# Optimization experiments

Hardware: AMD Instinct MI355X
Metric: run time of the kernel (lower is better)

Reference implementation:

```python
import jax, jax.numpy as jnp
import numpy as np

IN_DIM = 256
OUT_DIM = 256
EMBED_DIM = 256
GROUPS = 8
BN_EPS = 1e-5


def conv2d(x, w, b, pad, groups=1):
    # x: NCHW, w: OIHW (I = in_ch / groups)
    out = jax.lax.conv_general_dilated(
        x, w, window_strides=(1, 1), padding=[(pad, pad), (pad, pad)],
        dimension_numbers=('NCHW', 'OIHW', 'NCHW'), feature_group_count=groups)
    return out + b[None, :, None, None]


def setup_inputs() -> dict:
    key = jax.random.key(0)
    ks = jax.random.split(key, 8)
    s = 0.05
    d = {}
    d['x'] = jax.random.normal(ks[0], (2, IN_DIM, 16, 16), jnp.float32)
    d['y'] = jax.random.normal(ks[1], (2, OUT_DIM, 128, 128), jnp.float32)
    # channle_reduce: Conv2d(256, 64, k=3, groups=64) -> weight (64, 4, 3, 3)
    d['w_cr'] = jax.random.normal(ks[2], (IN_DIM // 4, 4, 3, 3), jnp.float32) * s
    d['b_cr'] = jnp.zeros((IN_DIM // 4,), jnp.float32)
    # depthwise convs on 64 channels
    d['w_dw3'] = jax.random.normal(ks[3], (IN_DIM // 4, 1, 3, 3), jnp.float32) * s
    d['b_dw3'] = jnp.zeros((IN_DIM // 4,), jnp.float32)
    d['w_dw7'] = jax.random.normal(ks[4], (IN_DIM // 4, 1, 5, 5), jnp.float32) * s
    d['b_dw7'] = jnp.zeros((IN_DIM // 4,), jnp.float32)
    # gate: Conv2d(256, 128, 1) + BN + StarReLU
    d['w_gate'] = jax.random.normal(ks[5], (IN_DIM // 2, IN_DIM, 1, 1), jnp.float32) * s
    d['b_gate'] = jnp.zeros((IN_DIM // 2,), jnp.float32)
    d['bn_gamma'] = jnp.ones((IN_DIM // 2,), jnp.float32)
    d['bn_beta'] = jnp.zeros((IN_DIM // 2,), jnp.float32)
    d['bn_mean'] = jnp.zeros((IN_DIM // 2,), jnp.float32)
    d['bn_var'] = jnp.ones((IN_DIM // 2,), jnp.float32)
    d['sr_scale'] = jnp.ones((1,), jnp.float32)
    d['sr_bias'] = jnp.zeros((1,), jnp.float32)
    # linear1: Linear(16, 8192) -> torch weight shape (8192, 16)
    d['w_lin'] = jax.random.normal(ks[6], (OUT_DIM * EMBED_DIM // GROUPS, IN_DIM // (2 * GROUPS)), jnp.float32) * s
    d['b_lin'] = jnp.zeros((OUT_DIM * EMBED_DIM // GROUPS,), jnp.float32)
    return d


def reference(x, y, w_cr, b_cr, w_dw3, b_dw3, w_dw7, b_dw7, w_gate, b_gate,
              bn_gamma, bn_beta, bn_mean, bn_var, sr_scale, sr_bias, w_lin, b_lin):
    B, C, H, Wd = x.shape
    # gate branch: 1x1 conv -> BN (inference stats) -> StarReLU
    g = conv2d(x, w_gate, b_gate, 0)
    inv = (bn_gamma / jnp.sqrt(bn_var + BN_EPS))[None, :, None, None]
    g = (g - bn_mean[None, :, None, None]) * inv + bn_beta[None, :, None, None]
    g = sr_scale * jnp.square(jnp.maximum(g, 0.0)) + sr_bias
    # feature branch
    xr = conv2d(x, w_cr, b_cr, 1, groups=IN_DIM // 4)        # (B, 64, H, W)
    x3 = conv2d(xr, w_dw3, b_dw3, 1, groups=IN_DIM // 4)
    x7 = conv2d(xr, w_dw7, b_dw7, 2, groups=IN_DIM // 4)
    xc = jnp.concatenate([x3, x7], axis=1) * g               # (B, 128, H, W)
    # per-pixel weight generation: (B,H,W,G,16) @ (16,8192)
    xc = xc.reshape(B, GROUPS, -1, H, Wd).transpose(0, 3, 4, 1, 2)
    wdec = jnp.einsum('bhwgi,oi->bhwgo', xc, w_lin) + b_lin  # (B,H,W,8,8192)
    # flatten (G, out*embed/G) -> (embed, out); matches torch reshape order
    wdec = wdec.reshape(B, H, Wd, EMBED_DIM, OUT_DIM)
    # patch-wise dynamic 1x1 conv == per-patch batched matmul
    b, c, h, w = y.shape
    fh, fw = H, Wd
    ph, pw = h // fh, w // fw
    yp = y.reshape(b, c, fh, ph, fw, pw)
    # out[b,e,f,p,g,q] = sum_c wdec[b,f,g,e,c] * y[b,c,f,p,g,q]
    out = jnp.einsum('bfgec,bcfpgq->befpgq', wdec, yp)
    return out.reshape(b, EMBED_DIM, h, w)
```

## Files before the change

### kernel.cpp

```cpp
#include <hip/hip_runtime.h>
#include <stdint.h>


typedef __attribute__((ext_vector_type(8))) short short8;
typedef __attribute__((ext_vector_type(4))) float f32x4;

#define BN_EPS 1e-5f

__device__ __forceinline__ unsigned short f2bf(float f) {
  unsigned u = __float_as_uint(f);
  return (unsigned short)((u + 0x8000u) >> 16);
}
__device__ __forceinline__ unsigned pk2bf(float a, float b) {
  unsigned ua = __float_as_uint(a), ub = __float_as_uint(b);
  return ((ua + 0x8000u) >> 16) | ((ub + 0x8000u) & 0xFFFF0000u);
}

__global__ __launch_bounds__(256) void k1_merged(
    const float* __restrict__ x, const float* __restrict__ w_cr,
    const float* __restrict__ b_cr, const float* __restrict__ w_dw3,
    const float* __restrict__ b_dw3, const float* __restrict__ w_dw7,
    const float* __restrict__ b_dw7, const float* __restrict__ w_gate,
    const float* __restrict__ b_gate, const float* __restrict__ bn_gamma,
    const float* __restrict__ bn_beta, const float* __restrict__ bn_mean,
    const float* __restrict__ bn_var, const float* __restrict__ sr_scale,
    const float* __restrict__ sr_bias, const float* __restrict__ w_lin,
    short* __restrict__ wlin_bf, float* __restrict__ f0_out,
    float* __restrict__ gs_out)
{
  __shared__ __align__(16) float xcen[256];
  __shared__ __align__(16) float xs[4][256];
  __shared__ __align__(16) float xrs[256];

  int blk = blockIdx.x;
  int t = threadIdx.x;

  if (blk < 512) {
    int b = blk >> 8, h = (blk >> 4) & 15, w = blk & 15;
    int pix = (b * 16 + h) * 16 + w;

    { int idx = blk * 256 + t; wlin_bf[idx] = (short)f2bf(w_lin[idx]); }

    xcen[t] = x[b * 65536 + t * 256 + h * 16 + w];
    __syncthreads();

    int wave = t >> 6, lane = t & 63;
    int oq = lane >> 2, ol = lane & 3;
    const float4* wg4 = (const float4*)w_gate;
    const float4* xc4 = (const float4*)xcen;
    float ss = sr_scale[0], sb = sr_bias[0];

    #pragma unroll
    for (int pass = 0; pass < 2; ++pass) {
      int o = wave * 32 + pass * 16 + oq;
      float acc = 0.f;
      #pragma unroll
      for (int k = 0; k < 16; ++k) {
        int j = k * 4 + ol;
        float4 wv = wg4[o * 64 + j];
        float4 xv = xc4[j];
        acc += wv.x * xv.x + wv.y * xv.y + wv.z * xv.z + wv.w * xv.w;
      }
      acc += __shfl_xor(acc, 1);
      acc += __shfl_xor(acc, 2);
      float inv = bn_gamma[o] * rsqrtf(bn_var[o] + BN_EPS);
      float gg = (acc + b_gate[o] - bn_mean[o]) * inv + bn_beta[o];
      gg = fmaxf(gg, 0.f);
      gg = ss * gg * gg + sb;
      if (ol == 0) gs_out[pix * 128 + o] = gg;
    }
  } else {
    int cb = blk - 512;
    int b = cb >> 6, cr = cb & 63;
    {
      int ch = t >> 6, off = (t & 63) * 4;
      float4 v = *(const float4*)(x + b * 65536 + (cr * 4 + ch) * 256 + off);
      *(float4*)&xs[ch][off] = v;
    }
    __syncthreads();
    int h = t >> 4, w = t & 15;
    float a = b_cr[cr];
    #pragma unroll
    for (int ii = 0; ii < 4; ++ii) {
      const float* wp = w_cr + (cr * 4 + ii) * 9;
      #pragma unroll
      for (int ky = 0; ky < 3; ++ky) {
        int gy = h + ky - 1;
        #pragma unroll
        for (int kx = 0; kx < 3; ++kx) {
          int gx = w + kx - 1;
          float v = (gy >= 0 && gy < 16 && gx >= 0 && gx < 16) ? xs[ii][gy * 16 + gx] : 0.f;
          a += wp[ky * 3 + kx] * v;
        }
      }
    }
    xrs[t] = a;
    __syncthreads();

    float f3 = b_dw3[cr];
    {
      const float* wp = w_dw3 + cr * 9;
      #pragma unroll
      for (int ky = 0; ky < 3; ++ky) {
        int gy = h + ky - 1;
        #pragma unroll
        for (int kx = 0; kx < 3; ++kx) {
          int gx = w + kx - 1;
          float v = (gy >= 0 && gy < 16 && gx >= 0 && gx < 16) ? xrs[gy * 16 + gx] : 0.f;
          f3 += wp[ky * 3 + kx] * v;
        }
      }
    }
    float f5 = b_dw7[cr];
    {
      const float* wp = w_dw7 + cr * 25;
      #pragma unroll
      for (int ky = 0; ky < 5; ++ky) {
        int gy = h + ky - 2;
        #pragma unroll
        for (int kx = 0; kx < 5; ++kx) {
          int gx = w + kx - 2;
          float v = (gy >= 0 && gy < 16 && gx >= 0 && gx < 16) ? xrs[gy * 16 + gx] : 0.f;
          f5 += wp[ky * 5 + kx] * v;
        }
      }
    }
    int pix = (b * 16 + h) * 16 + w;
    f0_out[pix * 128 + cr] = f3;
    f0_out[pix * 128 + 64 + cr] = f5;
  }
}

__global__ __launch_bounds__(512, 4) void k2_fused(
    const float* __restrict__ y, const short* __restrict__ wlin_bf,
    const float* __restrict__ f0_in, const float* __restrict__ gs_in,
    const float* __restrict__ b_lin, float* __restrict__ out)
{
  __shared__ __align__(16) short Ylds[16384];
  __shared__ __align__(16) char dyn[16640];
  float* scratch = (float*)dyn;
  short* wdbase = (short*)dyn;

  int phys = blockIdx.x;
  int blk = (phys & 7) * 64 + (phys >> 3);
  int b = blk >> 8, f = (blk >> 4) & 15, g = blk & 15;
  int tid = threadIdx.x;
  int wave = tid >> 6, lane = tid & 63;
  int quad = lane >> 4, l16 = lane & 15;
  int geff = l16 & 7, jsel = l16 >> 3;

  const float* yb = y + b * 4194304 + (f * 8) * 128 + g * 8;

  int c32 = tid >> 4, pf = tid & 15;
  float4 yv[2][2];
  #pragma unroll
  for (int s = 0; s < 2; ++s)
    #pragma unroll
    for (int it = 0; it < 2; ++it)
      yv[s][it] = *(const float4*)(yb + (s * 64 + it * 32 + c32) * 16384 + (pf >> 1) * 128 + (pf & 1) * 4);

  short8 aw[2][2][2];
  float4 bl[2][2][2];
  #pragma unroll
  for (int s = 0; s < 2; ++s)
    #pragma unroll
    for (int jj = 0; jj < 2; ++jj) {
      int jA = wave * 4 + jj * 2 + (quad >> 1);
      int jD = wave * 4 + jj * 2 + jsel;
      #pragma unroll
      for (int hh = 0; hh < 2; ++hh) {
        int c0 = s * 32 + hh * 16;
        aw[s][jj][hh] = *(const short8*)(wlin_bf + (jA * 256 + c0 + l16) * 16 + (quad & 1) * 8);
        bl[s][jj][hh] = *(const float4*)(b_lin + jD * 256 + c0 + quad * 4);
      }
    }

  bool bval = (jsel == (quad >> 1));
  const float* f0p = f0_in + blk * 128 + geff * 16 + (quad & 1) * 8;
  const float* gsp = gs_in + blk * 128 + geff * 16 + (quad & 1) * 8;
  float4 f0a = *(const float4*)f0p, f0b = *(const float4*)(f0p + 4);
  float4 gsa = *(const float4*)gsp, gsb = *(const float4*)(gsp + 4);

  #pragma unroll
  for (int sch = 0; sch < 4; ++sch) {
    #pragma unroll
    for (int it = 0; it < 2; ++it)
      *(float4*)&scratch[(it * 32 + c32) * 65 + pf * 4] = yv[sch & 1][it];
    if (sch < 2) {
      #pragma unroll
      for (int it = 0; it < 2; ++it)
        yv[sch & 1][it] = *(const float4*)(yb + ((sch + 2) * 64 + it * 32 + c32) * 16384 + (pf >> 1) * 128 + (pf & 1) * 4);
    }
    __syncthreads();
    {
      int pix = tid & 63, cg = tid >> 6;
      float s0 = scratch[(cg * 8 + 0) * 65 + pix];
      float s1 = scratch[(cg * 8 + 1) * 65 + pix];
      float s2 = scratch[(cg * 8 + 2) * 65 + pix];
      float s3 = scratch[(cg * 8 + 3) * 65 + pix];
      float s4 = scratch[(cg * 8 + 4) * 65 + pix];
      float s5 = scratch[(cg * 8 + 5) * 65 + pix];
      float s6 = scratch[(cg * 8 + 6) * 65 + pix];
      float s7 = scratch[(cg * 8 + 7) * 65 + pix];
      uint4 pk;
      pk.x = pk2bf(s0, s1); pk.y = pk2bf(s2, s3);
      pk.z = pk2bf(s4, s5); pk.w = pk2bf(s6, s7);
      int chunk = sch * 8 + cg;
      int physc = chunk ^ (pix & 15);
      *(uint4*)&Ylds[pix * 256 + physc * 8] = pk;
    }
    __syncthreads();
  }

  short8 bx = {0, 0, 0, 0, 0, 0, 0, 0};
  if (bval) {
    bx[0] = (short)f2bf(f0a.x * gsa.x); bx[1] = (short)f2bf(f0a.y * gsa.y);
    bx[2] = (short)f2bf(f0a.z * gsa.z); bx[3] = (short)f2bf(f0a.w * gsa.w);
    bx[4] = (short)f2bf(f0b.x * gsb.x); bx[5] = (short)f2bf(f0b.y * gsb.y);
    bx[6] = (short)f2bf(f0b.z * gsb.z); bx[7] = (short)f2bf(f0b.w * gsb.w);
  }

  f32x4 acc[2][4];
  #pragma unroll
  for (int et = 0; et < 2; ++et)
    #pragma unroll
    for (int nt = 0; nt < 4; ++nt)
      acc[et][nt] = {0.f, 0.f, 0.f, 0.f};

  short* wdw = wdbase + wave * 1024;

  auto gen_chunk = [&](int cc, int slot) {
    #pragma unroll
    for (int jj = 0; jj < 2; ++jj) {
      int ep = geff * 4 + jj * 2 + jsel;
      int gx = ((ep >> 2) & 3) ^ (ep & 3);
      #pragma unroll
      for (int hh = 0; hh < 2; ++hh) {
        float4 blv = bl[slot][jj][hh];
        f32x4 cin = {blv.x, blv.y, blv.z, blv.w};
        f32x4 d = __builtin_amdgcn_mfma_f32_16x16x32_bf16(aw[slot][jj][hh], bx, cin, 0, 0, 0);
        uint2 pk;
        pk.x = pk2bf(d[0], d[1]);
        pk.y = pk2bf(d[2], d[3]);
        int q16 = (hh * 2 + (quad >> 1)) ^ gx;
        *(uint2*)&wdw[ep * 32 + q16 * 8 + (quad & 1) * 4] = pk;
      }
    }
  };

  gen_chunk(0, 0);

  #pragma unroll
  for (int cc = 0; cc < 8; ++cc) {
    short8 A2[2], Bf[4];
    #pragma unroll
    for (int et = 0; et < 2; ++et) {
      int ep = (l16 & 7) * 4 + et * 2 + (l16 >> 3);
      int gx = ((ep >> 2) & 3) ^ (ep & 3);
      A2[et] = *(const short8*)&wdw[ep * 32 + (quad ^ gx) * 8];
    }
    int chunkY = cc * 4 + quad;
    #pragma unroll
    for (int nt = 0; nt < 4; ++nt) {
      int physc = chunkY ^ l16;
      Bf[nt] = *(const short8*)&Ylds[(nt * 16 + l16) * 256 + physc * 8];
    }
    if (cc < 6) {
      #pragma unroll
      for (int jj = 0; jj < 2; ++jj) {
        int jA = wave * 4 + jj * 2 + (quad >> 1);
        int jD = wave * 4 + jj * 2 + jsel;
        #pragma unroll
        for (int hh = 0; hh < 2; ++hh) {
          int c0 = (cc + 2) * 32 + hh * 16;
          aw[cc & 1][jj][hh] = *(const short8*)(wlin_bf + (jA * 256 + c0 + l16) * 16 + (quad & 1) * 8);
          bl[cc & 1][jj][hh] = *(const float4*)(b_lin + jD * 256 + c0 + quad * 4);
        }
      }
    }
    if (cc < 7) gen_chunk(cc + 1, (cc + 1) & 1);
    #pragma unroll
    for (int et = 0; et < 2; ++et)
      #pragma unroll
      for (int nt = 0; nt < 4; ++nt)
        acc[et][nt] = __builtin_amdgcn_mfma_f32_16x16x32_bf16(A2[et], Bf[nt], acc[et][nt], 0, 0, 0);
  }

  float* ob = out + b * 4194304 + (f * 8) * 128 + g * 8;
  #pragma unroll
  for (int et = 0; et < 2; ++et) {
    #pragma unroll
    for (int nt = 0; nt < 4; ++nt) {
      int pix = nt * 16 + l16;
      float* oa = ob + (pix >> 3) * 128 + (pix & 7);
      #pragma unroll
      for (int r = 0; r < 4; ++r) {
        int m = quad * 4 + r;
        int e = (m & 7) * 32 + wave * 4 + et * 2 + (m >> 3);
        oa[e * 16384] = acc[et][nt][r];
      }
    }
  }
}

extern "C" void kernel_launch(void* const* d_in, const int* in_sizes, int n_in,
                              void* d_out, int out_size, void* d_ws, size_t ws_size,
                              hipStream_t stream) {
  const float* x        = (const float*)d_in[0];
  const float* y        = (const float*)d_in[1];
  const float* w_cr     = (const float*)d_in[2];
  const float* b_cr     = (const float*)d_in[3];
  const float* w_dw3    = (const float*)d_in[4];
  const float* b_dw3    = (const float*)d_in[5];
  const float* w_dw7    = (const float*)d_in[6];
  const float* b_dw7    = (const float*)d_in[7];
  const float* w_gate   = (const float*)d_in[8];
  const float* b_gate   = (const float*)d_in[9];
  const float* bn_gamma = (const float*)d_in[10];
  const float* bn_beta  = (const float*)d_in[11];
  const float* bn_mean  = (const float*)d_in[12];
  const float* bn_var   = (const float*)d_in[13];
  const float* sr_scale = (const float*)d_in[14];
  const float* sr_bias  = (const float*)d_in[15];
  const float* w_lin    = (const float*)d_in[16];
  const float* b_lin    = (const float*)d_in[17];
  float* out = (float*)d_out;

  float* f0      = (float*)d_ws;
  float* gs      = (float*)((char*)d_ws + 262144);
  short* wlin_bf = (short*)((char*)d_ws + 524288);

  hipLaunchKernelGGL(k1_merged, dim3(640), dim3(256), 0, stream,
                     x, w_cr, b_cr, w_dw3, b_dw3, w_dw7, b_dw7, w_gate, b_gate,
                     bn_gamma, bn_beta, bn_mean, bn_var, sr_scale, sr_bias,
                     w_lin, wlin_bf, f0, gs);
  hipLaunchKernelGGL(k2_fused, dim3(512), dim3(512), 0, stream,
                     y, wlin_bf, f0, gs, b_lin, out);
}
```

Baseline: 152.6 us.

## Fuse prologue convs and gate into main kernel, convert w_lin to bf16 on the fly

Merges the first kernel (grouped conv, depthwise convs, gate conv with BN and StarReLU, w_lin bf16 conversion) into the main per-patch kernel. Each block now recomputes its own pixel's features from a 7x7 halo window of x held in LDS, and converts w_lin from fp32 to bf16 in registers just before each MFMA. This removes a kernel launch and the workspace round trip. In exchange it adds redundant per-block prologue compute, several extra barriers, twice as many bytes loaded for w_lin, and more register pressure.

New measurement: 183.8 us. 20.4% more time.

```diff
diff --git a/kernel.cpp b/kernel.cpp
--- a/kernel.cpp
+++ b/kernel.cpp
@@ -15,151 +15,153 @@
   unsigned ua = __float_as_uint(a), ub = __float_as_uint(b);
   return ((ua + 0x8000u) >> 16) | ((ub + 0x8000u) & 0xFFFF0000u);
 }
-
-__global__ __launch_bounds__(256) void k1_merged(
-    const float* __restrict__ x, const float* __restrict__ w_cr,
-    const float* __restrict__ b_cr, const float* __restrict__ w_dw3,
-    const float* __restrict__ b_dw3, const float* __restrict__ w_dw7,
-    const float* __restrict__ b_dw7, const float* __restrict__ w_gate,
-    const float* __restrict__ b_gate, const float* __restrict__ bn_gamma,
-    const float* __restrict__ bn_beta, const float* __restrict__ bn_mean,
-    const float* __restrict__ bn_var, const float* __restrict__ sr_scale,
-    const float* __restrict__ sr_bias, const float* __restrict__ w_lin,
-    short* __restrict__ wlin_bf, float* __restrict__ f0_out,
-    float* __restrict__ gs_out)
-{
-  __shared__ __align__(16) float xcen[256];
-  __shared__ __align__(16) float xs[4][256];
-  __shared__ __align__(16) float xrs[256];
-
-  int blk = blockIdx.x;
-  int t = threadIdx.x;
-
-  if (blk < 512) {
-    int b = blk >> 8, h = (blk >> 4) & 15, w = blk & 15;
-    int pix = (b * 16 + h) * 16 + w;
-
-    { int idx = blk * 256 + t; wlin_bf[idx] = (short)f2bf(w_lin[idx]); }
-
-    xcen[t] = x[b * 65536 + t * 256 + h * 16 + w];
-    __syncthreads();
-
-    int wave = t >> 6, lane = t & 63;
-    int oq = lane >> 2, ol = lane & 3;
-    const float4* wg4 = (const float4*)w_gate;
-    const float4* xc4 = (const float4*)xcen;
-    float ss = sr_scale[0], sb = sr_bias[0];
-
-    #pragma unroll
-    for (int pass = 0; pass < 2; ++pass) {
-      int o = wave * 32 + pass * 16 + oq;
-      float acc = 0.f;
-      #pragma unroll
-      for (int k = 0; k < 16; ++k) {
-        int j = k * 4 + ol;
-        float4 wv = wg4[o * 64 + j];
-        float4 xv = xc4[j];
-        acc += wv.x * xv.x + wv.y * xv.y + wv.z * xv.z + wv.w * xv.w;
-      }
-      acc += __shfl_xor(acc, 1);
-      acc += __shfl_xor(acc, 2);
-      float inv = bn_gamma[o] * rsqrtf(bn_var[o] + BN_EPS);
-      float gg = (acc + b_gate[o] - bn_mean[o]) * inv + bn_beta[o];
-      gg = fmaxf(gg, 0.f);
-      gg = ss * gg * gg + sb;
-      if (ol == 0) gs_out[pix * 128 + o] = gg;
-    }
-  } else {
-    int cb = blk - 512;
-    int b = cb >> 6, cr = cb & 63;
-    {
-      int ch = t >> 6, off = (t & 63) * 4;
-      float4 v = *(const float4*)(x + b * 65536 + (cr * 4 + ch) * 256 + off);
-      *(float4*)&xs[ch][off] = v;
-    }
-    __syncthreads();
-    int h = t >> 4, w = t & 15;
-    float a = b_cr[cr];
-    #pragma unroll
-    for (int ii = 0; ii < 4; ++ii) {
-      const float* wp = w_cr + (cr * 4 + ii) * 9;
-      #pragma unroll
-      for (int ky = 0; ky < 3; ++ky) {
-        int gy = h + ky - 1;
-        #pragma unroll
-        for (int kx = 0; kx < 3; ++kx) {
-          int gx = w + kx - 1;
-          float v = (gy >= 0 && gy < 16 && gx >= 0 && gx < 16) ? xs[ii][gy * 16 + gx] : 0.f;
-          a += wp[ky * 3 + kx] * v;
-        }
-      }
-    }
-    xrs[t] = a;
-    __syncthreads();
-
-    float f3 = b_dw3[cr];
-    {
-      const float* wp = w_dw3 + cr * 9;
-      #pragma unroll
-      for (int ky = 0; ky < 3; ++ky) {
-        int gy = h + ky - 1;
-        #pragma unroll
-        for (int kx = 0; kx < 3; ++kx) {
-          int gx = w + kx - 1;
-          float v = (gy >= 0 && gy < 16 && gx >= 0 && gx < 16) ? xrs[gy * 16 + gx] : 0.f;
-          f3 += wp[ky * 3 + kx] * v;
-        }
-      }
-    }
-    float f5 = b_dw7[cr];
-    {
-      const float* wp = w_dw7 + cr * 25;
-      #pragma unroll
-      for (int ky = 0; ky < 5; ++ky) {
-        int gy = h + ky - 2;
-        #pragma unroll
-        for (int kx = 0; kx < 5; ++kx) {
-          int gx = w + kx - 2;
-          float v = (gy >= 0 && gy < 16 && gx >= 0 && gx < 16) ? xrs[gy * 16 + gx] : 0.f;
-          f5 += wp[ky * 5 + kx] * v;
-        }
-      }
-    }
-    int pix = (b * 16 + h) * 16 + w;
-    f0_out[pix * 128 + cr] = f3;
-    f0_out[pix * 128 + 64 + cr] = f5;
-  }
-}
-
-__global__ __launch_bounds__(512, 4) void k2_fused(
-    const float* __restrict__ y, const short* __restrict__ wlin_bf,
-    const float* __restrict__ f0_in, const float* __restrict__ gs_in,
-    const float* __restrict__ b_lin, float* __restrict__ out)
+__device__ __forceinline__ short8 cvt8(float4 a, float4 b) {
+  union { uint4 u; short8 s; } r;
+  r.u.x = pk2bf(a.x, a.y); r.u.y = pk2bf(a.z, a.w);
+  r.u.z = pk2bf(b.x, b.y); r.u.w = pk2bf(b.z, b.w);
+  return r.s;
+}
+
+__global__ __launch_bounds__(512, 4) void k_fused(
+    const float* __restrict__ x, const float* __restrict__ y,
+    const float* __restrict__ w_cr, const float* __restrict__ b_cr,
+    const float* __restrict__ w_dw3, const float* __restrict__ b_dw3,
+    const float* __restrict__ w_dw7, const float* __restrict__ b_dw7,
+    const float* __restrict__ w_gate, const float* __restrict__ b_gate,
+    const float* __restrict__ bn_gamma, const float* __restrict__ bn_beta,
+    const float* __restrict__ bn_mean, const float* __restrict__ bn_var,
+    const float* __restrict__ sr_scale, const float* __restrict__ sr_bias,
+    const float* __restrict__ w_lin, const float* __restrict__ b_lin,
+    float* __restrict__ out)
 {
   __shared__ __align__(16) short Ylds[16384];
   __shared__ __align__(16) char dyn[16640];
+  float* xwf    = (float*)Ylds;
+  float* xcen   = (float*)dyn;
+  float* xrw    = (float*)(dyn + 1024);
+  float* f0buf  = (float*)(dyn + 4224);
+  float* gsbuf  = (float*)(dyn + 4736);
   float* scratch = (float*)dyn;
-  short* wdbase = (short*)dyn;
+  short* wdbase  = (short*)dyn;
 
   int phys = blockIdx.x;
   int blk = (phys & 7) * 64 + (phys >> 3);
-  int b = blk >> 8, f = (blk >> 4) & 15, g = blk & 15;
+  int b = blk >> 8, pf_ = (blk >> 4) & 15, pg_ = blk & 15;
   int tid = threadIdx.x;
   int wave = tid >> 6, lane = tid & 63;
   int quad = lane >> 4, l16 = lane & 15;
   int geff = l16 & 7, jsel = l16 >> 3;
 
-  const float* yb = y + b * 4194304 + (f * 8) * 128 + g * 8;
+  const float* yb = y + b * 4194304 + (pf_ * 8) * 128 + pg_ * 8;
 
   int c32 = tid >> 4, pf = tid & 15;
+  int pxo = (pf >> 1) * 128 + (pf & 1) * 4;
   float4 yv[2][2];
   #pragma unroll
   for (int s = 0; s < 2; ++s)
     #pragma unroll
     for (int it = 0; it < 2; ++it)
-      yv[s][it] = *(const float4*)(yb + (s * 64 + it * 32 + c32) * 16384 + (pf >> 1) * 128 + (pf & 1) * 4);
-
-  short8 aw[2][2][2];
+      yv[s][it] = *(const float4*)(yb + (s * 64 + it * 32 + c32) * 16384 + pxo);
+
+  if (tid < 256) xcen[tid] = x[b * 65536 + tid * 256 + pf_ * 16 + pg_];
+
+  for (int h2 = 0; h2 < 2; ++h2) {
+    for (int t2 = tid; t2 < 896; t2 += 512) {
+      int grp = t2 / 28;
+      int rem = t2 - grp * 28;
+      int ch = rem / 7, row = rem - (rem / 7) * 7;
+      int cg = (h2 * 32 + grp) * 4 + ch;
+      int gy = pf_ - 3 + row;
+      int gyc = min(max(gy, 0), 15);
+      const float* xrow = x + b * 65536 + cg * 256 + gyc * 16;
+      float* wrow = xwf + (grp * 4 + ch) * 49 + row * 7;
+      #pragma unroll
+      for (int kx = 0; kx < 7; ++kx) {
+        int gx = pg_ - 3 + kx;
+        int gxc = min(max(gx, 0), 15);
+        float v = xrow[gxc];
+        wrow[kx] = (gy >= 0 && gy < 16 && gx >= 0 && gx < 16) ? v : 0.f;
+      }
+    }
+    __syncthreads();
+    for (int t2 = tid; t2 < 800; t2 += 512) {
+      int grp = t2 / 25, pos = t2 - (t2 / 25) * 25;
+      int py = pos / 5, px = pos - (pos / 5) * 5;
+      int cr = h2 * 32 + grp;
+      int xy = pf_ - 2 + py, xx = pg_ - 2 + px;
+      float v = 0.f;
+      if (xy >= 0 && xy < 16 && xx >= 0 && xx < 16) {
+        v = b_cr[cr];
+        #pragma unroll
+        for (int ii = 0; ii < 4; ++ii) {
+          const float* wp = w_cr + (cr * 4 + ii) * 9;
+          const float* xw = xwf + (grp * 4 + ii) * 49;
+          #pragma unroll
+          for (int ky = 0; ky < 3; ++ky)
+            #pragma unroll
+            for (int kx = 0; kx < 3; ++kx)
+              v += wp[ky * 3 + kx] * xw[(py + ky) * 7 + (px + kx)];
+        }
+      }
+      xrw[grp * 25 + pos] = v;
+    }
+    __syncthreads();
+    if (tid < 64) {
+      int grp = tid >> 1, which = tid & 1, cr = h2 * 32 + grp;
+      const float* xr0 = xrw + grp * 25;
+      if (which == 0) {
+        float v = b_dw3[cr];
+        const float* wp = w_dw3 + cr * 9;
+        #pragma unroll
+        for (int ky = 0; ky < 3; ++ky)
+          #pragma unroll
+          for (int kx = 0; kx < 3; ++kx)
+            v += wp[ky * 3 + kx] * xr0[(ky + 1) * 5 + (kx + 1)];
+        f0buf[cr] = v;
+      } else {
+        float v = b_dw7[cr];
+        const float* wp = w_dw7 + cr * 25;
+        #pragma unroll
+        for (int ky = 0; ky < 5; ++ky)
+          #pragma unroll
+          for (int kx = 0; kx < 5; ++kx)
+            v += wp[ky * 5 + kx] * xr0[ky * 5 + kx];
+        f0buf[64 + cr] = v;
+      }
+    }
+    __syncthreads();
+  }
+
+  {
+    int o = tid >> 2, ol = tid & 3;
+    const float4* wg4 = (const float4*)w_gate;
+    const float4* xc4 = (const float4*)xcen;
+    float acc = 0.f;
+    #pragma unroll
+    for (int k = 0; k < 16; ++k) {
+      int j = k * 4 + ol;
+      float4 wv = wg4[o * 64 + j];
+      float4 xv = xc4[j];
+      acc += wv.x * xv.x + wv.y * xv.y + wv.z * xv.z + wv.w * xv.w;
+    }
+    acc += __shfl_xor(acc, 1);
+    acc += __shfl_xor(acc, 2);
+    float inv = bn_gamma[o] * rsqrtf(bn_var[o] + BN_EPS);
+    float gg = (acc + b_gate[o] - bn_mean[o]) * inv + bn_beta[o];
+    gg = fmaxf(gg, 0.f);
+    gg = sr_scale[0] * gg * gg + sr_bias[0];
+    if (ol == 0) gsbuf[o] = gg;
+  }
+  __syncthreads();
+
+  bool bval = (jsel == (quad >> 1));
+  const float* f0p = f0buf + geff * 16 + (quad & 1) * 8;
+  const float* gsp = gsbuf + geff * 16 + (quad & 1) * 8;
+  float4 f0a = *(const float4*)f0p, f0b = *(const float4*)(f0p + 4);
+  float4 gsa = *(const float4*)gsp, gsb = *(const float4*)(gsp + 4);
+  __syncthreads();
+
+  float4 awf[2][2][2][2];
   float4 bl[2][2][2];
   #pragma unroll
   for (int s = 0; s < 2; ++s)
@@ -170,16 +172,12 @@
       #pragma unroll
       for (int hh = 0; hh < 2; ++hh) {
         int c0 = s * 32 + hh * 16;
-        aw[s][jj][hh] = *(const short8*)(wlin_bf + (jA * 256 + c0 + l16) * 16 + (quad & 1) * 8);
+        const float* wp = w_lin + (jA * 256 + c0 + l16) * 16 + (quad & 1) * 8;
+        awf[s][jj][hh][0] = *(const float4*)wp;
+        awf[s][jj][hh][1] = *(const float4*)(wp + 4);
         bl[s][jj][hh] = *(const float4*)(b_lin + jD * 256 + c0 + quad * 4);
       }
     }
-
-  bool bval = (jsel == (quad >> 1));
-  const float* f0p = f0_in + blk * 128 + geff * 16 + (quad & 1) * 8;
-  const float* gsp = gs_in + blk * 128 + geff * 16 + (quad & 1) * 8;
-  float4 f0a = *(const float4*)f0p, f0b = *(const float4*)(f0p + 4);
-  float4 gsa = *(const float4*)gsp, gsb = *(const float4*)(gsp + 4);
 
   #pragma unroll
   for (int sch = 0; sch < 4; ++sch) {
@@ -189,7 +187,7 @@
     if (sch < 2) {
       #pragma unroll
       for (int it = 0; it < 2; ++it)
-        yv[sch & 1][it] = *(const float4*)(yb + ((sch + 2) * 64 + it * 32 + c32) * 16384 + (pf >> 1) * 128 + (pf & 1) * 4);
+        yv[sch & 1][it] = *(const float4*)(yb + ((sch + 2) * 64 + it * 32 + c32) * 16384 + pxo);
     }
     __syncthreads();
     {
@@ -238,7 +236,8 @@
       for (int hh = 0; hh < 2; ++hh) {
         float4 blv = bl[slot][jj][hh];
         f32x4 cin = {blv.x, blv.y, blv.z, blv.w};
-        f32x4 d = __builtin_amdgcn_mfma_f32_16x16x32_bf16(aw[slot][jj][hh], bx, cin, 0, 0, 0);
+        short8 aws = cvt8(awf[slot][jj][hh][0], awf[slot][jj][hh][1]);
+        f32x4 d = __builtin_amdgcn_mfma_f32_16x16x32_bf16(aws, bx, cin, 0, 0, 0);
         uint2 pk;
         pk.x = pk2bf(d[0], d[1]);
         pk.y = pk2bf(d[2], d[3]);
@@ -273,7 +272,9 @@
         #pragma unroll
         for (int hh = 0; hh < 2; ++hh) {
           int c0 = (cc + 2) * 32 + hh * 16;
-          aw[cc & 1][jj][hh] = *(const short8*)(wlin_bf + (jA * 256 + c0 + l16) * 16 + (quad & 1) * 8);
+          const float* wp = w_lin + (jA * 256 + c0 + l16) * 16 + (quad & 1) * 8;
+          awf[cc & 1][jj][hh][0] = *(const float4*)wp;
+          awf[cc & 1][jj][hh][1] = *(const float4*)(wp + 4);
           bl[cc & 1][jj][hh] = *(const float4*)(b_lin + jD * 256 + c0 + quad * 4);
         }
       }
@@ -286,7 +287,7 @@
         acc[et][nt] = __builtin_amdgcn_mfma_f32_16x16x32_bf16(A2[et], Bf[nt], acc[et][nt], 0, 0, 0);
   }
 
-  float* ob = out + b * 4194304 + (f * 8) * 128 + g * 8;
+  float* ob = out + b * 4194304 + (pf_ * 8) * 128 + pg_ * 8;
   #pragma unroll
   for (int et = 0; et < 2; ++et) {
     #pragma unroll
@@ -326,14 +327,8 @@
   const float* b_lin    = (const float*)d_in[17];
   float* out = (float*)d_out;
 
-  float* f0      = (float*)d_ws;
-  float* gs      = (float*)((char*)d_ws + 262144);
-  short* wlin_bf = (short*)((char*)d_ws + 524288);
-
-  hipLaunchKernelGGL(k1_merged, dim3(640), dim3(256), 0, stream,
-                     x, w_cr, b_cr, w_dw3, b_dw3, w_dw7, b_dw7, w_gate, b_gate,
-                     bn_gamma, bn_beta, bn_mean, bn_var, sr_scale, sr_bias,
-                     w_lin, wlin_bf, f0, gs);
-  hipLaunchKernelGGL(k2_fused, dim3(512), dim3(512), 0, stream,
-                     y, wlin_bf, f0, gs, b_lin, out);
-}
+  hipLaunchKernelGGL(k_fused, dim3(512), dim3(512), 0, stream,
+                     x, y, w_cr, b_cr, w_dw3, b_dw3, w_dw7, b_dw7,
+                     w_gate, b_gate, bn_gamma, bn_beta, bn_mean, bn_var,
+                     sr_scale, sr_bias, w_lin, b_lin, out);
+}
```
